# Kernel optimization log

Measured on AMD Instinct MI355X. Metric: run time of the kernel, lower is better.

## Reference

```python
import jax, jax.numpy as jnp
import numpy as np

N_NODES = 100000
N_EDGES = 1600000
H_FEATS = 128
HIDDEN = 32


def setup_inputs() -> dict:
    key = jax.random.key(0)
    k_h, k_src, k_dst, k_w1, k_w2 = jax.random.split(key, 5)
    h = jax.random.normal(k_h, (N_NODES, H_FEATS), dtype=jnp.float32)
    src = jax.random.randint(k_src, (N_EDGES,), 0, N_NODES, dtype=jnp.int64 if jax.config.jax_enable_x64 else jnp.int32)
    dst = jax.random.randint(k_dst, (N_EDGES,), 0, N_NODES, dtype=jnp.int64 if jax.config.jax_enable_x64 else jnp.int32)
    # Linear weights (PyTorch default init scale ~ 1/sqrt(fan_in))
    W1 = jax.random.normal(k_w1, (H_FEATS, HIDDEN), dtype=jnp.float32) / np.sqrt(H_FEATS)
    b1 = jnp.zeros((HIDDEN,), dtype=jnp.float32)
    W2 = jax.random.normal(k_w2, (HIDDEN, 1), dtype=jnp.float32) / np.sqrt(HIDDEN)
    b2 = jnp.zeros((1,), dtype=jnp.float32)
    return {"h": h, "src": src, "dst": dst, "W1": W1, "b1": b1, "W2": W2, "b2": b2}


def reference(h, src, dst, W1, b1, W2, b2):
    # gather src/dst node features per edge and multiply elementwise: [E, F]
    he = h[src] * h[dst]
    # 2-layer MLP score: [E]
    hidden = jax.nn.relu(he @ W1 + b1)          # [E, 32]
    score = (hidden @ W2 + b2)[:, 0]            # [E]
    return score
```

## Files before the change

### kernel.cpp

```cpp
#include <hip/hip_runtime.h>
#include <hip/hip_bf16.h>
#include <hip/hip_fp16.h>

#define H_FEATS 128
#define HIDDEN  32
#define BUCKET_SHIFT 9
#define MAX_BUCKETS 1024
#define SORT_EPB 4096

typedef _Float16 f16x8 __attribute__((ext_vector_type(8)));
typedef float    f32x4 __attribute__((ext_vector_type(4)));

union H8 { uint4 u; __half2 h2[4]; };
union U16 { uint4 u; f16x8 h; };

__device__ __forceinline__ void do_convert_h(
    const float* __restrict__ h, __half* __restrict__ hh, int i, int n8)
{
    if (i >= n8) return;
    const float4* s = reinterpret_cast<const float4*>(h) + (size_t)i * 2;
    float4 a = s[0], b = s[1];
    H8 r;
    r.h2[0] = __floats2half2_rn(a.x, a.y);
    r.h2[1] = __floats2half2_rn(a.z, a.w);
    r.h2[2] = __floats2half2_rn(b.x, b.y);
    r.h2[3] = __floats2half2_rn(b.z, b.w);
    reinterpret_cast<uint4*>(hh)[i] = r.u;
}

__global__ __launch_bounds__(256) void prep_fused_kernel(
    const float* __restrict__ h, __half* __restrict__ hh, int n8,
    const float* __restrict__ W1, __half* __restrict__ w1t,
    const int* __restrict__ src, int* __restrict__ blockhist,
    int n_edges, int nbuck, int hb, int cb, int wb)
{
    __shared__ int lh[MAX_BUCKETS];
    int bid = blockIdx.x;
    int tid = threadIdx.x;

    if (bid < cb) {
        do_convert_h(h, hh, bid * 256 + tid, n8);
        return;
    }
    bid -= cb;
    if (bid < wb) {
        int t = bid * 256 + tid;
        if (t < H_FEATS * HIDDEN) {
            int k = t >> 5, n = t & 31;
            w1t[(size_t)n * H_FEATS + k] = __float2half(W1[t]);
        }
        return;
    }
    bid -= wb;
    for (int i = tid; i < nbuck; i += 256) lh[i] = 0;
    __syncthreads();
    int ebase = bid * SORT_EPB;
#pragma unroll
    for (int k = 0; k < SORT_EPB / 256; ++k) {
        int e = ebase + k * 256 + tid;
        if (e < n_edges) atomicAdd(&lh[src[e] >> BUCKET_SHIFT], 1);
    }
    __syncthreads();
    for (int i = tid; i < nbuck; i += 256)
        blockhist[(size_t)i * hb + bid] = lh[i];
}

__global__ __launch_bounds__(256) void convert_h_kernel(
    const float* __restrict__ h, __half* __restrict__ hh, int n8)
{
    do_convert_h(h, hh, blockIdx.x * blockDim.x + threadIdx.x, n8);
}

__global__ __launch_bounds__(256) void scan_rows_kernel(
    int* __restrict__ blockhist, int* __restrict__ rowsum, int nblocks)
{
    __shared__ int tmp[256];
    int row = blockIdx.x;
    int tid = threadIdx.x;
    size_t rowbase = (size_t)row * nblocks;
    int carry = 0;
    for (int c = 0; c < nblocks; c += 256) {
        int idx = c + tid;
        int v = (idx < nblocks) ? blockhist[rowbase + idx] : 0;
        tmp[tid] = v;
        __syncthreads();
#pragma unroll
        for (int d = 1; d < 256; d <<= 1) {
            int t = (tid >= d) ? tmp[tid - d] : 0;
            __syncthreads();
            tmp[tid] += t;
            __syncthreads();
        }
        int incl = tmp[tid];
        if (idx < nblocks) blockhist[rowbase + idx] = carry + incl - v;
        carry += tmp[255];
        __syncthreads();
    }
    if (tid == 0) rowsum[row] = carry;
}

__global__ __launch_bounds__(MAX_BUCKETS) void scan_base_kernel(
    const int* __restrict__ rowsum, int* __restrict__ base, int nbuck)
{
    __shared__ int tmp[MAX_BUCKETS];
    int tid = threadIdx.x;
    int v = (tid < nbuck) ? rowsum[tid] : 0;
    tmp[tid] = v;
    __syncthreads();
#pragma unroll
    for (int d = 1; d < MAX_BUCKETS; d <<= 1) {
        int t = (tid >= d) ? tmp[tid - d] : 0;
        __syncthreads();
        tmp[tid] += t;
        __syncthreads();
    }
    if (tid < nbuck) base[tid] = tmp[tid] - v;
}

__global__ __launch_bounds__(256) void scatter_kernel(
    const int* __restrict__ src, const int* __restrict__ dst,
    const int* __restrict__ blockhist, const int* __restrict__ base,
    int2* __restrict__ spair, int* __restrict__ seid,
    int n_edges, int nbuck, int nblocks)
{
    __shared__ int lcur[MAX_BUCKETS];
    int tid = threadIdx.x;
    for (int i = tid; i < nbuck; i += 256)
        lcur[i] = base[i] + blockhist[(size_t)i * nblocks + blockIdx.x];
    __syncthreads();
    int ebase = blockIdx.x * SORT_EPB;
#pragma unroll
    for (int k = 0; k < SORT_EPB / 256; ++k) {
        int e = ebase + k * 256 + tid;
        if (e < n_edges) {
            int s = src[e];
            int p = atomicAdd(&lcur[s >> BUCKET_SHIFT], 1);
            spair[p] = make_int2(s, dst[e]);
            seid[p] = e;
        }
    }
}

__device__ __forceinline__ void issue_g(
    const __half* __restrict__ hh, int2 sp, int koff, U16 (&A)[4], U16 (&B)[4])
{
    const __half* hs = hh + (size_t)sp.x * H_FEATS;
    const __half* hd = hh + (size_t)sp.y * H_FEATS;
#pragma unroll
    for (int s = 0; s < 4; ++s) {
        A[s].u = *reinterpret_cast<const uint4*>(hs + s * 32 + koff);
        B[s].u = *reinterpret_cast<const uint4*>(hd + s * 32 + koff);
    }
}

__device__ __forceinline__ void compute_g(
    U16 (&A)[4], U16 (&B)[4], const f16x8 (&w1frag)[2][4],
    const float* b1lop, const float* b1hip, const float* w2lop, const float* w2hip,
    float b2f, int kq, int sid, bool eok, float* __restrict__ out)
{
    f32x4 acc0 = {0.f, 0.f, 0.f, 0.f};
    f32x4 acc1 = {0.f, 0.f, 0.f, 0.f};
#pragma unroll
    for (int s = 0; s < 4; ++s) {
        f16x8 he = A[s].h * B[s].h;
        acc0 = __builtin_amdgcn_mfma_f32_16x16x32_f16(w1frag[0][s], he, acc0, 0, 0, 0);
        acc1 = __builtin_amdgcn_mfma_f32_16x16x32_f16(w1frag[1][s], he, acc1, 0, 0, 0);
    }
    float p = 0.f;
#pragma unroll
    for (int r = 0; r < 4; ++r) {
        float h0 = acc0[r] + b1lop[r]; h0 = h0 > 0.f ? h0 : 0.f;
        float h1 = acc1[r] + b1hip[r]; h1 = h1 > 0.f ? h1 : 0.f;
        p = fmaf(h0, w2lop[r], p);
        p = fmaf(h1, w2hip[r], p);
    }
    p += __shfl_xor(p, 16, 64);
    p += __shfl_xor(p, 32, 64);
    if (kq == 0 && eok) out[sid] = p + b2f;
}

__global__ __launch_bounds__(256, 2) void edge_mlp_mfma_kernel(
    const __half* __restrict__ hh,
    const __half* __restrict__ w1t,
    const int2*  __restrict__ spair,
    const int*   __restrict__ seid,
    const float* __restrict__ b1,
    const float* __restrict__ W2,
    const float* __restrict__ b2,
    float*       __restrict__ out,
    int n_edges, int nblocks)
{
    int bid = blockIdx.x;
    int q8 = nblocks >> 3, r8 = nblocks & 7;
    int xcd = bid & 7, idx = bid >> 3;
    int chunk = (xcd < r8) ? (xcd * (q8 + 1) + idx)
                           : (r8 * (q8 + 1) + (xcd - r8) * q8 + idx);
    int tile = chunk * 256;

    int lane = (int)(threadIdx.x & 63);
    int wv   = (int)(threadIdx.x >> 6);
    int m    = lane & 15;
    int kq   = lane >> 4;
    int koff = kq * 8;

    f16x8 w1frag[2][4];
#pragma unroll
    for (int nt = 0; nt < 2; ++nt)
#pragma unroll
        for (int s = 0; s < 4; ++s) {
            U16 t;
            t.u = *reinterpret_cast<const uint4*>(
                w1t + (size_t)(nt * 16 + m) * H_FEATS + s * 32 + koff);
            w1frag[nt][s] = t.h;
        }

    float4 b1lo = *reinterpret_cast<const float4*>(b1 + kq * 4);
    float4 b1hi = *reinterpret_cast<const float4*>(b1 + 16 + kq * 4);
    float4 w2lo = *reinterpret_cast<const float4*>(W2 + kq * 4);
    float4 w2hi = *reinterpret_cast<const float4*>(W2 + 16 + kq * 4);
    const float* b1lop = reinterpret_cast<const float*>(&b1lo);
    const float* b1hip = reinterpret_cast<const float*>(&b1hi);
    const float* w2lop = reinterpret_cast<const float*>(&w2lo);
    const float* w2hip = reinterpret_cast<const float*>(&w2hi);
    float b2f = b2[0];

    int base = tile + wv * 64;

    int e0 = base + m,      e1 = base + 16 + m;
    int e2 = base + 32 + m, e3 = base + 48 + m;
    bool ok0 = e0 < n_edges, ok1 = e1 < n_edges, ok2 = e2 < n_edges, ok3 = e3 < n_edges;
    int2 sp0 = spair[ok0 ? e0 : n_edges - 1];
    int2 sp1 = spair[ok1 ? e1 : n_edges - 1];
    int2 sp2 = spair[ok2 ? e2 : n_edges - 1];
    int2 sp3 = spair[ok3 ? e3 : n_edges - 1];
    int sid0 = seid[ok0 ? e0 : n_edges - 1];
    int sid1 = seid[ok1 ? e1 : n_edges - 1];
    int sid2 = seid[ok2 ? e2 : n_edges - 1];
    int sid3 = seid[ok3 ? e3 : n_edges - 1];

    U16 xA[4], xB[4];
    U16 yA[4], yB[4];
    U16 zA[4], zB[4];

    issue_g(hh, sp0, koff, xA, xB);
    issue_g(hh, sp1, koff, yA, yB);
    issue_g(hh, sp2, koff, zA, zB);
    __builtin_amdgcn_sched_barrier(0);
    compute_g(xA, xB, w1frag, b1lop, b1hip, w2lop, w2hip, b2f, kq, sid0, ok0, out);
    __builtin_amdgcn_sched_barrier(0);
    issue_g(hh, sp3, koff, xA, xB);
    __builtin_amdgcn_sched_barrier(0);
    compute_g(yA, yB, w1frag, b1lop, b1hip, w2lop, w2hip, b2f, kq, sid1, ok1, out);
    __builtin_amdgcn_sched_barrier(0);
    compute_g(zA, zB, w1frag, b1lop, b1hip, w2lop, w2hip, b2f, kq, sid2, ok2, out);
    __builtin_amdgcn_sched_barrier(0);
    compute_g(xA, xB, w1frag, b1lop, b1hip, w2lop, w2hip, b2f, kq, sid3, ok3, out);
}

__global__ __launch_bounds__(256) void edge_mlp_fp16_kernel(
    const __half* __restrict__ hh,
    const int*   __restrict__ src,
    const int*   __restrict__ dst,
    const float* __restrict__ W1,
    const float* __restrict__ b1,
    const float* __restrict__ W2,
    const float* __restrict__ b2,
    float*       __restrict__ out,
    int n_edges)
{
    int e = blockIdx.x * blockDim.x + threadIdx.x;
    if (e >= n_edges) return;

    const __half* hs = hh + (size_t)src[e] * H_FEATS;
    const __half* hd = hh + (size_t)dst[e] * H_FEATS;

    float hidden[HIDDEN];
#pragma unroll
    for (int j = 0; j < HIDDEN; ++j) hidden[j] = b1[j];

#pragma unroll 2
    for (int f0 = 0; f0 < H_FEATS; f0 += 8) {
        H8 A, B;
        A.u = *reinterpret_cast<const uint4*>(hs + f0);
        B.u = *reinterpret_cast<const uint4*>(hd + f0);
        float he[8];
#pragma unroll
        for (int k = 0; k < 4; ++k) {
            float2 a = __half22float2(A.h2[k]);
            float2 b = __half22float2(B.h2[k]);
            he[2 * k]     = a.x * b.x;
            he[2 * k + 1] = a.y * b.y;
        }
        const float* w = W1 + (size_t)f0 * HIDDEN;
#pragma unroll
        for (int j = 0; j < HIDDEN; ++j) {
            float acc = hidden[j];
#pragma unroll
            for (int k = 0; k < 8; ++k)
                acc = fmaf(he[k], w[(size_t)k * HIDDEN + j], acc);
            hidden[j] = acc;
        }
    }

    float score = b2[0];
#pragma unroll
    for (int j = 0; j < HIDDEN; ++j) {
        float r = hidden[j] > 0.0f ? hidden[j] : 0.0f;
        score = fmaf(r, W2[j], score);
    }
    out[e] = score;
}

__global__ __launch_bounds__(256) void edge_mlp_kernel(
    const float* __restrict__ h,
    const int*   __restrict__ src,
    const int*   __restrict__ dst,
    const float* __restrict__ W1,
    const float* __restrict__ b1,
    const float* __restrict__ W2,
    const float* __restrict__ b2,
    float*       __restrict__ out,
    int n_edges)
{
    int e = blockIdx.x * blockDim.x + threadIdx.x;
    if (e >= n_edges) return;

    const float* hs = h + (size_t)src[e] * H_FEATS;
    const float* hd = h + (size_t)dst[e] * H_FEATS;

    float hidden[HIDDEN];
#pragma unroll
    for (int j = 0; j < HIDDEN; ++j) hidden[j] = b1[j];

#pragma unroll 4
    for (int f0 = 0; f0 < H_FEATS; f0 += 4) {
        float4 a = *reinterpret_cast<const float4*>(hs + f0);
        float4 b = *reinterpret_cast<const float4*>(hd + f0);
        float he0 = a.x * b.x, he1 = a.y * b.y, he2 = a.z * b.z, he3 = a.w * b.w;
        const float* w0 = W1 + (size_t)(f0 + 0) * HIDDEN;
        const float* w1 = W1 + (size_t)(f0 + 1) * HIDDEN;
        const float* w2 = W1 + (size_t)(f0 + 2) * HIDDEN;
        const float* w3 = W1 + (size_t)(f0 + 3) * HIDDEN;
#pragma unroll
        for (int j = 0; j < HIDDEN; ++j) {
            float acc = hidden[j];
            acc = fmaf(he0, w0[j], acc);
            acc = fmaf(he1, w1[j], acc);
            acc = fmaf(he2, w2[j], acc);
            acc = fmaf(he3, w3[j], acc);
            hidden[j] = acc;
        }
    }

    float score = b2[0];
#pragma unroll
    for (int j = 0; j < HIDDEN; ++j) {
        float r = hidden[j] > 0.0f ? hidden[j] : 0.0f;
        score = fmaf(r, W2[j], score);
    }
    out[e] = score;
}

extern "C" void kernel_launch(void* const* d_in, const int* in_sizes, int n_in,
                              void* d_out, int out_size, void* d_ws, size_t ws_size,
                              hipStream_t stream) {
    const float* h   = (const float*)d_in[0];
    const int*   src = (const int*)  d_in[1];
    const int*   dst = (const int*)  d_in[2];
    const float* W1  = (const float*)d_in[3];
    const float* b1  = (const float*)d_in[4];
    const float* W2  = (const float*)d_in[5];
    const float* b2  = (const float*)d_in[6];
    float* out = (float*)d_out;

    int n_node_feats = in_sizes[0];
    int n_edges = in_sizes[1];
    int n_nodes = n_node_feats / H_FEATS;
    int nbuck = (n_nodes + (1 << BUCKET_SHIFT) - 1) >> BUCKET_SHIFT;

    const int block = 256;
    int egrid  = (n_edges + block - 1) / block;
    int sgrid  = (n_edges + SORT_EPB - 1) / SORT_EPB;

    size_t hh_bytes  = (size_t)n_node_feats * sizeof(__half);
    size_t off_w1t   = (hh_bytes + 255) & ~(size_t)255;
    size_t off_spair = (off_w1t + (size_t)H_FEATS * HIDDEN * 2 + 255) & ~(size_t)255;
    size_t off_seid  = off_spair + (size_t)n_edges * 8;
    size_t off_bh    = off_seid + (size_t)n_edges * 4;
    size_t off_rsum  = off_bh + (size_t)nbuck * sgrid * 4;
    size_t off_base  = off_rsum + (size_t)MAX_BUCKETS * 4;
    size_t need_full = off_base + (size_t)MAX_BUCKETS * 4;

    int n8 = n_node_feats / 8;

    if (ws_size >= need_full && nbuck <= MAX_BUCKETS) {
        char* ws = (char*)d_ws;
        __half* hh     = (__half*)ws;
        __half* w1t    = (__half*)(ws + off_w1t);
        int2*   spair  = (int2*)(ws + off_spair);
        int*    seid   = (int*)(ws + off_seid);
        int*    blockhist = (int*)(ws + off_bh);
        int*    rowsum = (int*)(ws + off_rsum);
        int*    base   = (int*)(ws + off_base);

        int cb = (n8 + block - 1) / block;
        int wb = (H_FEATS * HIDDEN + block - 1) / block;
        int hb = sgrid;
        prep_fused_kernel<<<cb + wb + hb, block, 0, stream>>>(
            h, hh, n8, W1, w1t, src, blockhist, n_edges, nbuck, hb, cb, wb);
        scan_rows_kernel<<<nbuck, block, 0, stream>>>(blockhist, rowsum, sgrid);
        scan_base_kernel<<<1, MAX_BUCKETS, 0, stream>>>(rowsum, base, nbuck);
        scatter_kernel<<<sgrid, block, 0, stream>>>(src, dst, blockhist, base,
                                                    spair, seid,
                                                    n_edges, nbuck, sgrid);
        edge_mlp_mfma_kernel<<<egrid, block, 0, stream>>>(hh, w1t, spair, seid,
                                                          b1, W2, b2, out,
                                                          n_edges, egrid);
    } else if (ws_size >= hh_bytes) {
        __half* hh = (__half*)d_ws;
        convert_h_kernel<<<(n8 + block - 1) / block, block, 0, stream>>>(h, hh, n8);
        edge_mlp_fp16_kernel<<<egrid, block, 0, stream>>>(hh, src, dst,
                                                          W1, b1, W2, b2, out, n_edges);
    } else {
        edge_mlp_kernel<<<egrid, block, 0, stream>>>(h, src, dst,
                                                     W1, b1, W2, b2, out, n_edges);
    }
}
```

Before: 171.2 us.

## Add second-level subsort of edges by exact source node within buckets

Adds a per-bucket counting sort that orders edges by the low 9 bits of the source index inside each 512-node bucket. The edge MLP kernel then reads edges grouped by exact source node, so consecutive edges reuse the same source row and cache locality for the gather improves. This costs an extra kernel launch, another pass over the edge pairs and ids, and extra workspace for a second copy of those buffers, and it only runs when the workspace is large enough.

```diff
diff --git a/kernel.cpp b/kernel.cpp
--- a/kernel.cpp
+++ b/kernel.cpp
@@ -138,6 +138,49 @@
             spair[p] = make_int2(s, dst[e]);
             seid[p] = e;
         }
+    }
+}
+
+__global__ __launch_bounds__(256) void subsort_kernel(
+    const int2* __restrict__ spair1, const int* __restrict__ seid1,
+    const int* __restrict__ base, const int* __restrict__ rowsum,
+    int2* __restrict__ spair2, int* __restrict__ seid2)
+{
+    __shared__ int lh[512];
+    __shared__ int lcur[512];
+    __shared__ int tmp[256];
+    int b = blockIdx.x;
+    int tid = threadIdx.x;
+    int start = base[b];
+    int cnt = rowsum[b];
+
+    for (int i = tid; i < 512; i += 256) lh[i] = 0;
+    __syncthreads();
+    for (int i = tid; i < cnt; i += 256)
+        atomicAdd(&lh[spair1[start + i].x & 511], 1);
+    __syncthreads();
+
+    int v0 = lh[2 * tid], v1 = lh[2 * tid + 1];
+    tmp[tid] = v0 + v1;
+    __syncthreads();
+#pragma unroll
+    for (int d = 1; d < 256; d <<= 1) {
+        int t = (tid >= d) ? tmp[tid - d] : 0;
+        __syncthreads();
+        tmp[tid] += t;
+        __syncthreads();
+    }
+    int excl = tmp[tid] - (v0 + v1);
+    lcur[2 * tid] = excl;
+    lcur[2 * tid + 1] = excl + v0;
+    __syncthreads();
+
+    for (int i = tid; i < cnt; i += 256) {
+        int2 sp = spair1[start + i];
+        int sid = seid1[start + i];
+        int p = atomicAdd(&lcur[sp.x & 511], 1);
+        spair2[start + p] = sp;
+        seid2[start + p] = sid;
     }
 }
 
@@ -382,18 +425,21 @@
     int egrid  = (n_edges + block - 1) / block;
     int sgrid  = (n_edges + SORT_EPB - 1) / SORT_EPB;
 
-    size_t hh_bytes  = (size_t)n_node_feats * sizeof(__half);
-    size_t off_w1t   = (hh_bytes + 255) & ~(size_t)255;
-    size_t off_spair = (off_w1t + (size_t)H_FEATS * HIDDEN * 2 + 255) & ~(size_t)255;
-    size_t off_seid  = off_spair + (size_t)n_edges * 8;
-    size_t off_bh    = off_seid + (size_t)n_edges * 4;
-    size_t off_rsum  = off_bh + (size_t)nbuck * sgrid * 4;
-    size_t off_base  = off_rsum + (size_t)MAX_BUCKETS * 4;
-    size_t need_full = off_base + (size_t)MAX_BUCKETS * 4;
+    size_t hh_bytes   = (size_t)n_node_feats * sizeof(__half);
+    size_t off_w1t    = (hh_bytes + 255) & ~(size_t)255;
+    size_t off_spair  = (off_w1t + (size_t)H_FEATS * HIDDEN * 2 + 255) & ~(size_t)255;
+    size_t off_seid   = off_spair + (size_t)n_edges * 8;
+    size_t off_bh     = off_seid + (size_t)n_edges * 4;
+    size_t off_rsum   = off_bh + (size_t)nbuck * sgrid * 4;
+    size_t off_base   = off_rsum + (size_t)MAX_BUCKETS * 4;
+    size_t need_1lvl  = off_base + (size_t)MAX_BUCKETS * 4;
+    size_t off_spair2 = (need_1lvl + 255) & ~(size_t)255;
+    size_t off_seid2  = off_spair2 + (size_t)n_edges * 8;
+    size_t need_2lvl  = off_seid2 + (size_t)n_edges * 4;
 
     int n8 = n_node_feats / 8;
 
-    if (ws_size >= need_full && nbuck <= MAX_BUCKETS) {
+    if (ws_size >= need_1lvl && nbuck <= MAX_BUCKETS) {
         char* ws = (char*)d_ws;
         __half* hh     = (__half*)ws;
         __half* w1t    = (__half*)(ws + off_w1t);
@@ -413,9 +459,19 @@
         scatter_kernel<<<sgrid, block, 0, stream>>>(src, dst, blockhist, base,
                                                     spair, seid,
                                                     n_edges, nbuck, sgrid);
-        edge_mlp_mfma_kernel<<<egrid, block, 0, stream>>>(hh, w1t, spair, seid,
-                                                          b1, W2, b2, out,
-                                                          n_edges, egrid);
+        if (ws_size >= need_2lvl) {
+            int2* spair2 = (int2*)(ws + off_spair2);
+            int*  seid2  = (int*)(ws + off_seid2);
+            subsort_kernel<<<nbuck, block, 0, stream>>>(spair, seid, base, rowsum,
+                                                        spair2, seid2);
+            edge_mlp_mfma_kernel<<<egrid, block, 0, stream>>>(hh, w1t, spair2, seid2,
+                                                              b1, W2, b2, out,
+                                                              n_edges, egrid);
+        } else {
+            edge_mlp_mfma_kernel<<<egrid, block, 0, stream>>>(hh, w1t, spair, seid,
+                                                              b1, W2, b2, out,
+                                                              n_edges, egrid);
+        }
     } else if (ws_size >= hh_bytes) {
         __half* hh = (__half*)d_ws;
         convert_h_kernel<<<(n8 + block - 1) / block, block, 0, stream>>>(h, hh, n8);
```

Result: slower. 176.3 us (+3.0%).
